# Optimization experiments

Hardware: AMD Instinct MI355X
Metric: run time of the kernel (lower is better)

The kernel has to match this reference:

```python
import jax, jax.numpy as jnp
import numpy as np

NEG = jnp.float32(-1e9)
N_PRE = 12000   # n_train_pre_nms (module default training=True)
N_POST = 2000   # n_train_post_nms
MIN_SIZE = 16.0
NMS_THRESH = 0.7


def _make_anchors(feat_size=64, stride=16):
    scales = np.array([128.0, 256.0, 512.0])
    ratios = np.array([0.5, 1.0, 2.0])
    ws = (scales[:, None] * np.sqrt(1.0 / ratios)[None, :]).reshape(-1)  # [9]
    hs = (scales[:, None] * np.sqrt(ratios)[None, :]).reshape(-1)        # [9]
    ctr = (np.arange(feat_size) + 0.5) * stride
    cy, cx = np.meshgrid(ctr, ctr, indexing='ij')
    cx = cx.reshape(-1, 1); cy = cy.reshape(-1, 1)                       # [4096,1]
    x1 = cx - 0.5 * ws[None, :]; y1 = cy - 0.5 * hs[None, :]
    x2 = cx + 0.5 * ws[None, :]; y2 = cy + 0.5 * hs[None, :]
    return np.stack([x1, y1, x2, y2], axis=-1).reshape(-1, 4).astype(np.float32)  # [36864,4]


def setup_inputs() -> dict:
    key = jax.random.key(0)
    k1, k2 = jax.random.split(key)
    anchors = jnp.asarray(_make_anchors())[None]            # [1, 36864, 4]
    B, N = 8, anchors.shape[1]
    pred_loc = jax.random.normal(k1, (B, N, 4), jnp.float32) * 0.2
    pred_obj = jax.random.normal(k2, (B, N, 2), jnp.float32)
    return {"img_height": 1024, "img_width": 1024,
            "anchor_boxes": anchors, "pred_loc": pred_loc, "pred_obj": pred_obj}


def _decode(anchors, loc, img_w, img_h):
    # anchors [N,4] (x1,y1,x2,y2), loc [N,4] (dx,dy,dw,dh)
    w = anchors[:, 2] - anchors[:, 0]
    h = anchors[:, 3] - anchors[:, 1]
    cx = anchors[:, 0] + 0.5 * w
    cy = anchors[:, 1] + 0.5 * h
    pcx = loc[:, 0] * w + cx
    pcy = loc[:, 1] * h + cy
    pw = jnp.exp(loc[:, 2]) * w
    ph = jnp.exp(loc[:, 3]) * h
    x1 = jnp.clip(pcx - 0.5 * pw, 0.0, img_w)
    y1 = jnp.clip(pcy - 0.5 * ph, 0.0, img_h)
    x2 = jnp.clip(pcx + 0.5 * pw, 0.0, img_w)
    y2 = jnp.clip(pcy + 0.5 * ph, 0.0, img_h)
    return jnp.stack([x1, y1, x2, y2], axis=-1)  # [N,4]


def _iou_one_vs_all(box, boxes):
    # box [4], boxes [M,4]
    ix1 = jnp.maximum(box[0], boxes[:, 0])
    iy1 = jnp.maximum(box[1], boxes[:, 1])
    ix2 = jnp.minimum(box[2], boxes[:, 2])
    iy2 = jnp.minimum(box[3], boxes[:, 3])
    inter = jnp.maximum(ix2 - ix1, 0.0) * jnp.maximum(iy2 - iy1, 0.0)
    a0 = (box[2] - box[0]) * (box[3] - box[1])
    a1 = (boxes[:, 2] - boxes[:, 0]) * (boxes[:, 3] - boxes[:, 1])
    return inter / jnp.maximum(a0 + a1 - inter, 1e-9)


def _greedy_nms(boxes, scores):
    # boxes [M,4], scores [M] (invalid entries already NEG). Selects the first
    # N_POST boxes kept by greedy IoU suppression (exactly torchvision nms +
    # [:n_post] truncation, since greedy NMS emits in descending-score order).
    def step(s, _):
        i = jnp.argmax(s)
        valid = s[i] > NEG * 0.5
        box = boxes[i]
        suppress = _iou_one_vs_all(box, boxes) > NMS_THRESH  # includes self
        s = jnp.where(suppress, NEG, s)
        return s, (box, valid)
    _, (kept, mask) = jax.lax.scan(step, scores, None, length=N_POST)
    return jnp.where(mask[:, None], kept, 0.0), mask  # [N_POST,4], [N_POST]


def reference(img_height, img_width, anchor_boxes, pred_loc, pred_obj):
    img_h = jnp.float32(img_height)
    img_w = jnp.float32(img_width)
    anchors = anchor_boxes[0]                                    # [N,4]
    scores = jax.nn.softmax(pred_obj, axis=2)[:, :, 1]           # [B,N]
    boxes = jax.vmap(lambda l: _decode(anchors, l, img_w, img_h))(pred_loc)  # [B,N,4]
    # min-size filter -> mask scores instead of dynamic filtering
    valid = jnp.all(boxes[..., 2:] - boxes[..., :2] >= MIN_SIZE, axis=-1)    # [B,N]
    scores = jnp.where(valid, scores, NEG)
    # descending sort + pre-NMS truncation == top_k
    top_s, top_i = jax.lax.top_k(scores, N_PRE)                  # [B,N_PRE]
    top_boxes = jnp.take_along_axis(boxes, top_i[..., None], axis=1)         # [B,N_PRE,4]
    kept_boxes, kept_mask = jax.vmap(_greedy_nms)(top_boxes, top_s)
    return kept_boxes, kept_mask  # [B,N_POST,4] padded, [B,N_POST] validity
```

## Files before the change

### kernel.cpp

```cpp
#include <hip/hip_runtime.h>

typedef unsigned long long u64;
typedef unsigned int u32;

#define B_SZ   8
#define N_ANC  36864
#define N_PRE  12000
#define N_POST 2000
#define SEG    2048
#define NSEG   6
#define MAXC   (SEG * NSEG)
#define NW     (SEG / 64)
#define NDW    (MAXC / 64)
#define NBLK   144

__device__ __forceinline__ float area_of(float4 p) {
  return __fmul_rn(__fsub_rn(p.z, p.x), __fsub_rn(p.w, p.y));
}

__device__ __forceinline__ bool iou_gt_a(float4 p, float4 q, float a0, float a1) {
  float ix1 = fmaxf(p.x, q.x), iy1 = fmaxf(p.y, q.y);
  float ix2 = fminf(p.z, q.z), iy2 = fminf(p.w, q.w);
  float iw = fmaxf(__fsub_rn(ix2, ix1), 0.0f);
  float ih = fmaxf(__fsub_rn(iy2, iy1), 0.0f);
  float inter = __fmul_rn(iw, ih);
  float den = fmaxf(__fsub_rn(__fadd_rn(a0, a1), inter), 1e-9f);
  return (inter / den) > 0.7f;
}

__device__ __forceinline__ void block_sync_lgkm() {
  __builtin_amdgcn_sched_barrier(0);
  asm volatile("s_waitcnt lgkmcnt(0)" ::: "memory");
  __builtin_amdgcn_s_barrier();
  __builtin_amdgcn_sched_barrier(0);
}

__global__ __launch_bounds__(256) void k_decode(
    const int* __restrict__ imh_p, const int* __restrict__ imw_p,
    const float* __restrict__ anchors, const float* __restrict__ loc,
    const float* __restrict__ obj, float4* __restrict__ boxes,
    u64* __restrict__ keys, u32* __restrict__ hist)
{
  __shared__ u32 lh[2048];
  int t = threadIdx.x;
#pragma unroll
  for (int i = 0; i < 8; ++i) lh[t + i * 256] = 0;
  __syncthreads();

  int n = blockIdx.x * 256 + t;
  int b = blockIdx.y;
  float a0 = anchors[n * 4 + 0], a1 = anchors[n * 4 + 1];
  float a2 = anchors[n * 4 + 2], a3 = anchors[n * 4 + 3];
  size_t off = (size_t)b * N_ANC + n;
  float l0 = loc[off * 4 + 0], l1 = loc[off * 4 + 1];
  float l2 = loc[off * 4 + 2], l3 = loc[off * 4 + 3];

  float w  = __fsub_rn(a2, a0);
  float h  = __fsub_rn(a3, a1);
  float cx = __fadd_rn(a0, __fmul_rn(0.5f, w));
  float cy = __fadd_rn(a1, __fmul_rn(0.5f, h));
  float pcx = __fadd_rn(__fmul_rn(l0, w), cx);
  float pcy = __fadd_rn(__fmul_rn(l1, h), cy);
  float pw  = __fmul_rn(expf(l2), w);
  float ph  = __fmul_rn(expf(l3), h);
  float imw = (float)imw_p[0], imh = (float)imh_p[0];
  float hx = __fmul_rn(0.5f, pw), hy = __fmul_rn(0.5f, ph);
  float x1 = fminf(fmaxf(__fsub_rn(pcx, hx), 0.0f), imw);
  float y1 = fminf(fmaxf(__fsub_rn(pcy, hy), 0.0f), imh);
  float x2 = fminf(fmaxf(__fadd_rn(pcx, hx), 0.0f), imw);
  float y2 = fminf(fmaxf(__fadd_rn(pcy, hy), 0.0f), imh);
  boxes[off] = make_float4(x1, y1, x2, y2);

  bool valid = (__fsub_rn(x2, x1) >= 16.0f) && (__fsub_rn(y2, y1) >= 16.0f);

  float o0 = obj[off * 2 + 0], o1 = obj[off * 2 + 1];
  float m  = fmaxf(o0, o1);
  float e0 = expf(__fsub_rn(o0, m));
  float e1 = expf(__fsub_rn(o1, m));
  float s  = e1 / __fadd_rn(e0, e1);
  float sc = valid ? s : -1e9f;

  u32 u  = __float_as_uint(sc);
  u32 fk = (u & 0x80000000u) ? ~u : (u | 0x80000000u);
  u32 sk = ~fk;
  u64 key = ((u64)sk << 32) | (u32)n;
  keys[off] = key;
  atomicAdd(&lh[(u32)(key >> 53)], 1u);
  __syncthreads();
#pragma unroll
  for (int i = 0; i < 8; ++i) {
    u32 v = lh[t + i * 256];
    if (v) atomicAdd(&hist[b * 2048 + t + i * 256], v);
  }
}

__global__ __launch_bounds__(256) void k_pick1(
    const u32* __restrict__ hist, u32* __restrict__ T1, u32* __restrict__ Base1)
{
  int b = blockIdx.x, t = threadIdx.x;
  const u32* h = hist + b * 2048;
  __shared__ u32 part[256], pre[256];
  u32 loc[8], s = 0;
#pragma unroll
  for (int i = 0; i < 8; ++i) { loc[i] = h[t * 8 + i]; s += loc[i]; }
  part[t] = s;
  __syncthreads();
  if (t == 0) { u32 acc = 0; for (int i = 0; i < 256; ++i) { pre[i] = acc; acc += part[i]; } }
  __syncthreads();
  u32 acc = pre[t];
#pragma unroll
  for (int i = 0; i < 8; ++i) {
    u32 na = acc + loc[i];
    if (acc < N_PRE && na >= N_PRE) { T1[b] = (u32)(t * 8 + i); Base1[b] = acc; }
    acc = na;
  }
}

__global__ __launch_bounds__(256) void k_hist2(
    const u64* __restrict__ keys, const u32* __restrict__ T1,
    u32* __restrict__ hist)
{
  int b = blockIdx.y;
  u32 t1 = T1[b];
  __shared__ u32 lh[2048];
  int t = threadIdx.x;
#pragma unroll
  for (int i = 0; i < 8; ++i) lh[t + i * 256] = 0;
  __syncthreads();
#pragma unroll
  for (int k = 0; k < 4; ++k) {
    int i = blockIdx.x * 1024 + k * 256 + t;
    u64 key = keys[(size_t)b * N_ANC + i];
    if ((u32)(key >> 53) == t1) atomicAdd(&lh[(u32)(key >> 42) & 0x7FFu], 1u);
  }
  __syncthreads();
#pragma unroll
  for (int i = 0; i < 8; ++i) {
    u32 v = lh[t + i * 256];
    if (v) atomicAdd(&hist[b * 2048 + t + i * 256], v);
  }
}

__global__ __launch_bounds__(256) void k_pick2(
    const u32* __restrict__ hist, const u32* __restrict__ T1,
    const u32* __restrict__ Base1, u32* __restrict__ T2)
{
  int b = blockIdx.x, t = threadIdx.x;
  const u32* h = hist + b * 2048;
  __shared__ u32 part[256], pre[256];
  u32 loc[8], s = 0;
#pragma unroll
  for (int i = 0; i < 8; ++i) { loc[i] = h[t * 8 + i]; s += loc[i]; }
  part[t] = s;
  __syncthreads();
  if (t == 0) { u32 acc = Base1[b]; for (int i = 0; i < 256; ++i) { pre[i] = acc; acc += part[i]; } }
  __syncthreads();
  u32 acc = pre[t];
#pragma unroll
  for (int i = 0; i < 8; ++i) {
    u32 na = acc + loc[i];
    if (acc < N_PRE && na >= N_PRE) T2[b] = (T1[b] << 11) | (u32)(t * 8 + i);
    acc = na;
  }
}

__global__ __launch_bounds__(256) void k_count(
    const u64* __restrict__ keys, const u32* __restrict__ T2,
    u32* __restrict__ bcnt)
{
  int b = blockIdx.y;
  int i = blockIdx.x * 256 + threadIdx.x;
  u64 key = keys[(size_t)b * N_ANC + i];
  bool pred = (u32)(key >> 42) <= T2[b];
  u64 bal = __ballot(pred);
  __shared__ u32 wc[4];
  int wv = threadIdx.x >> 6, lane = threadIdx.x & 63;
  if (lane == 0) wc[wv] = (u32)__popcll(bal);
  __syncthreads();
  if (threadIdx.x == 0)
    bcnt[b * NBLK + blockIdx.x] = wc[0] + wc[1] + wc[2] + wc[3];
}

__global__ __launch_bounds__(256) void k_scatter(
    const u64* __restrict__ keys, const u32* __restrict__ T2,
    const u32* __restrict__ bcnt, u64* __restrict__ cand)
{
  int b = blockIdx.y, bx = blockIdx.x;
  int t = threadIdx.x;
  __shared__ u32 cnts[NBLK];
  __shared__ u32 wc[4];
  __shared__ u32 sbase;
  if (t < NBLK) cnts[t] = bcnt[b * NBLK + t];
  u64 key = keys[(size_t)b * N_ANC + bx * 256 + t];
  bool pred = (u32)(key >> 42) <= T2[b];
  u64 bal = __ballot(pred);
  int wv = t >> 6, lane = t & 63;
  if (lane == 0) wc[wv] = (u32)__popcll(bal);
  __syncthreads();
  if (t == 0) { u32 a = 0; for (int i = 0; i < bx; ++i) a += cnts[i]; sbase = a; }
  __syncthreads();
  u32 base = sbase;
  for (int w = 0; w < wv; ++w) base += wc[w];
  u32 rank = (u32)__popcll(bal & ((1ull << lane) - 1ull));
  if (pred) {
    u32 pos = base + rank;
    if (pos < MAXC) cand[(size_t)b * MAXC + pos] = key;
  }
}

#define SIDX(x) ((x) + ((x) >> 5))
__global__ __launch_bounds__(1024) void k_sort_tile(u64* __restrict__ a)
{
  int b = blockIdx.y, base = blockIdx.x * 2048;
  u64* p = a + (size_t)b * MAXC + base;
  __shared__ u64 lds[2048 + 64];
  int t = threadIdx.x;
  lds[SIDX(t)] = p[t];
  lds[SIDX(t + 1024)] = p[t + 1024];
  __syncthreads();
  for (int k = 2; k <= 2048; k <<= 1) {
    for (int j = k >> 1; j > 0; j >>= 1) {
      int i = ((t & ~(j - 1)) << 1) | (t & (j - 1));
      int l = i | j;
      bool asc = ((i & k) == 0);
      u64 x = lds[SIDX(i)], y = lds[SIDX(l)];
      if ((x > y) == asc) { lds[SIDX(i)] = y; lds[SIDX(l)] = x; }
      __syncthreads();
    }
  }
  p[t] = lds[SIDX(t)];
  p[t + 1024] = lds[SIDX(t + 1024)];
}

__global__ __launch_bounds__(256) void k_merge_gather(
    const u64* __restrict__ cand, const float4* __restrict__ boxes,
    float4* __restrict__ gbox, u64* __restrict__ deadm)
{
  int b = blockIdx.y;
  int p = blockIdx.x * 256 + threadIdx.x;
  const u64* cb = cand + (size_t)b * MAXC;
  u64 key = cb[p];
  int r = p >> 11;
  int rank = p & 2047;
#pragma unroll
  for (int s = 0; s < NSEG; ++s) {
    if (s == r) continue;
    const u64* run = cb + (s << 11);
    int lo = 0;
#pragma unroll
    for (int step = 2048; step >= 1; step >>= 1) {
      int np = lo + step;
      if (np <= 2048 && run[np - 1] < key) lo = np;
    }
    rank += lo;
  }
  bool valid = ((u32)(key >> 32) < 0x80000000u) && (rank < N_PRE);
  float4 bx = make_float4(0.f, 0.f, 0.f, 0.f);
  if (valid) bx = boxes[(size_t)b * N_ANC + (u32)key];
  gbox[(size_t)b * MAXC + rank] = bx;
  if (!valid) atomicOr(&deadm[b * NDW + (rank >> 6)], 1ull << (rank & 63));
}

__device__ __forceinline__ void segmask_tile(
    int b, int sg, int tile, const float4* __restrict__ gbox,
    u64* __restrict__ smask, u64* __restrict__ smaskT,
    float4* rbox, float* rarea, u64* diag)
{
  int r = tile, rg = 0;
  while (r >= 32 - rg) { r -= 32 - rg; ++rg; }
  int cw = rg + r;
  const float4* gb = gbox + (size_t)b * MAXC + sg * SEG;
  int t = threadIdx.x;
  if (t < 64) { float4 bx = gb[rg * 64 + t]; rbox[t] = bx; rarea[t] = area_of(bx); }
  __syncthreads();
  int wv = t >> 6, lane = t & 63;
  u64* srow = smask + (size_t)(b * NSEG + sg) * SEG * NW + (size_t)rg * 64 * NW;
  float4 cb4 = gb[cw * 64 + lane];
  float ca = area_of(cb4);
  bool isdiag = (cw == rg);
  for (int rr = wv * 16; rr < wv * 16 + 16; ++rr) {
    bool p = iou_gt_a(rbox[rr], cb4, rarea[rr], ca);
    if (isdiag) p = p && (lane > rr);
    u64 m = __ballot(p);
    if (lane == 0) { srow[(size_t)rr * NW + cw] = m; if (isdiag) diag[rr] = m; }
  }
  if (isdiag) {
    __syncthreads();
    if (t < 64) {
      u64 s = 0;
      for (int q = 0; q < 64; ++q) s |= ((diag[q] >> t) & 1ull) << q;
      smaskT[(size_t)(b * NSEG + sg) * SEG + rg * 64 + t] = s;
    }
  }
}

__global__ __launch_bounds__(256) void k_segmask01(
    const float4* __restrict__ gbox, u64* __restrict__ smask,
    u64* __restrict__ smaskT)
{
  __shared__ float4 rbox[64]; __shared__ float rarea[64]; __shared__ u64 diag[64];
  int b = blockIdx.y;
  int sg = blockIdx.x / 528, tile = blockIdx.x % 528;
  segmask_tile(b, sg, tile, gbox, smask, smaskT, rbox, rarea, diag);
}

__device__ __forceinline__ void cross_work(
    int b, int sg, int bx, const float4* __restrict__ gbox,
    const float4* __restrict__ keptb, const int* __restrict__ meta,
    u64* __restrict__ deadm, float4* kb, float* ka)
{
  int kc = bx >> 3, cbk = bx & 7;
  int nkept = meta[b * 8 + 0];
  int kbase = kc * 256;
  if (kbase >= nkept) return;
  int kcnt = min(256, nkept - kbase);
  int t = threadIdx.x;
  if (t < kcnt) {
    float4 k4 = keptb[(size_t)b * SEG + kbase + t];
    kb[t] = k4; ka[t] = area_of(k4);
  }
  __syncthreads();
  int gi = sg * SEG + cbk * 256 + t;
  float4 my = gbox[(size_t)b * MAXC + gi];
  float ma = area_of(my);
  bool sup = false;
  for (int kk = 0; kk < kcnt; ++kk) {
    if (iou_gt_a(kb[kk], my, ka[kk], ma)) { sup = true; break; }
  }
  u64 bm = __ballot(sup);
  if ((t & 63) == 0 && bm) atomicOr(&deadm[b * NDW + (gi >> 6)], bm);
}

__global__ __launch_bounds__(256) void k_cross(
    const float4* __restrict__ gbox, const float4* __restrict__ keptb,
    const int* __restrict__ meta, u64* __restrict__ deadm, int sg)
{
  int b = blockIdx.y;
  if (meta[b * 8 + 1]) return;
  __shared__ float4 kb[256]; __shared__ float ka[256];
  cross_work(b, sg, blockIdx.x, gbox, keptb, meta, deadm, kb, ka);
}

__global__ __launch_bounds__(256) void k_crossmask(
    const float4* __restrict__ gbox, const float4* __restrict__ keptb,
    const int* __restrict__ meta, u64* __restrict__ deadm,
    u64* __restrict__ smask, u64* __restrict__ smaskT, int sg)
{
  int b = blockIdx.y;
  if (meta[b * 8 + 1]) return;
  __shared__ float4 kb[256]; __shared__ float ka[256]; __shared__ u64 diag[64];
  if (blockIdx.x < 64) {
    cross_work(b, sg, blockIdx.x, gbox, keptb, meta, deadm, kb, ka);
  } else {
    segmask_tile(b, sg, blockIdx.x - 64, gbox, smask, smaskT,
                 kb, ka, diag);
  }
}

__global__ __launch_bounds__(1024) void k_walk(
    const float4* __restrict__ gbox, const u64* __restrict__ smask,
    const u64* __restrict__ smaskT, const u64* __restrict__ deadm,
    int* __restrict__ meta, float4* __restrict__ keptb,
    float* __restrict__ out, int sg)
{
  int b = blockIdx.x;
  if (meta[b * 8 + 1]) return;
  int t = threadIdx.x, wv = t >> 6, lane = t & 63;

  __shared__ u64 rowbuf[2][2048];
  __shared__ u64 stbuf[2][64];
  __shared__ float4 bbox[2][64];
  __shared__ u64 sdead[2];
  __shared__ u32 remv[64];
  __shared__ u32 klist[64];
  __shared__ int s_stop, s_nkept, s_kcnt;

  const u64* smb = smask + (size_t)(b * NSEG + sg) * SEG * NW;
  const u64* stb = smaskT + (size_t)(b * NSEG + sg) * SEG;
  const u64* dmb = deadm + b * NDW + sg * NW;
  const float4* gb = gbox + (size_t)b * MAXC + sg * SEG;
  float4* kbuf = keptb + (size_t)b * SEG;
  float4* ob = (float4*)(out + (size_t)b * N_POST * 4);
  float* om = out + (size_t)B_SZ * N_POST * 4 + (size_t)b * N_POST;

  {
    u64 a = smb[t], c = smb[t + 1024];
    u64 st_ = 0; float4 bb_ = make_float4(0.f, 0.f, 0.f, 0.f);
    if (t < 64) { st_ = stb[t]; bb_ = gb[t]; }
    u64 sd_ = (t == 0) ? dmb[0] : 0;
    rowbuf[0][t] = a;
    rowbuf[0][t + 1024] = c;
    if (t < 64) { stbuf[0][t] = st_; bbox[0][t] = bb_; remv[t] = 0; }
    if (t == 0) { sdead[0] = sd_; s_stop = 0; s_nkept = meta[b * 8 + 0]; }
  }
  int p0 = t - 64, p1 = p0 + 960, p2 = p0 + 1920;
  u64 Aa = 0, Ac = 0, Ae = 0, Ast = 0, Asd = 0;
  u64 Ba = 0, Bc = 0, Be = 0, Bst = 0, Bsd = 0;
  float4 Abb = make_float4(0.f, 0.f, 0.f, 0.f);
  float4 Bbb = make_float4(0.f, 0.f, 0.f, 0.f);
  if (wv > 0) {
    { const u64* src = smb + 2048;
      Aa = src[p0]; Ac = src[p1]; if (p0 < 128) Ae = src[p2];
      if (p0 < 64) { Ast = stb[64 + p0]; Abb = gb[64 + p0]; }
      if (t == 64) Asd = dmb[1]; }
    { const u64* src = smb + 2 * 2048;
      Ba = src[p0]; Bc = src[p1]; if (p0 < 128) Be = src[p2];
      if (p0 < 64) { Bst = stb[128 + p0]; Bbb = gb[128 + p0]; }
      if (t == 64) Bsd = dmb[2]; }
  }
  block_sync_lgkm();

  for (int g = 0; g < NW; ++g) {
    int cb = g & 1, nb = cb ^ 1;
    if (wv > 0) {
      bool useA = ((g & 1) == 0);
      if (g < NW - 1) {
        u64 wa = useA ? Aa : Ba, wc2 = useA ? Ac : Bc, we = useA ? Ae : Be;
        u64 wst = useA ? Ast : Bst, wsd = useA ? Asd : Bsd;
        float4 wbb = useA ? Abb : Bbb;
        rowbuf[nb][p0] = wa;
        rowbuf[nb][p1] = wc2;
        if (p0 < 128) rowbuf[nb][p2] = we;
        if (p0 < 64) { stbuf[nb][p0] = wst; bbox[nb][p0] = wbb; }
        if (t == 64) sdead[nb] = wsd;
      }
      if (g < NW - 3) {
        const u64* src = smb + (size_t)(g + 3) * 2048;
        u64 la = src[p0], lc = src[p1], le = (p0 < 128) ? src[p2] : 0;
        u64 lst = 0, lsd = 0;
        float4 lbb = make_float4(0.f, 0.f, 0.f, 0.f);
        if (p0 < 64) { lst = stb[(g + 3) * 64 + p0]; lbb = gb[(g + 3) * 64 + p0]; }
        if (t == 64) lsd = dmb[g + 3];
        if (useA) { Aa = la; Ac = lc; Ae = le; Ast = lst; Abb = lbb; Asd = lsd; }
        else      { Ba = la; Bc = lc; Be = le; Bst = lst; Bbb = lbb; Bsd = lsd; }
      }
    } else {
      int l = lane;
      u64 S = stbuf[cb][l];
      u64 remg = ((u64)remv[2 * g + 1] << 32) | remv[2 * g];
      u64 avail = ~(remg | sdead[cb]);
      u64 km = 0;
      while (avail) {
        bool al = (avail >> l) & 1;
        u64 newk = __ballot(al && (S & avail) == 0ull);
        u64 nd   = __ballot(al && (S & newk) != 0ull);
        km |= newk;
        avail &= ~(newk | nd);
      }
      int nk0 = s_nkept;
      int rem = N_POST - nk0;
      int kc = __popcll(km);
      bool stop = (kc >= rem);
      int rank = __popcll(km & ((1ull << l) - 1ull));
      if (((km >> l) & 1) && rank < rem) {
        float4 bx = bbox[cb][l];
        kbuf[nk0 + rank] = bx;
        ob[nk0 + rank] = bx;
        om[nk0 + rank] = 1.0f;
        klist[rank] = (u32)l;
      }
      if (l == 0) {
        int eff = stop ? rem : kc;
        s_kcnt = eff;
        s_nkept = nk0 + eff;
        if (stop) s_stop = 1;
      }
    }
    block_sync_lgkm();
    if (s_stop) break;
    if (g < NW - 1) {
      int kcnt = s_kcnt;
      if (kcnt) {
        u32* rb32 = (u32*)rowbuf[cb];
        for (int i = t; i < kcnt * 64; i += 1024) {
          int kk = i >> 6, w = i & 63;
          if ((w >> 1) > g) {
            u32 v = rb32[klist[kk] * 64 + w];
            if (v) atomicOr(&remv[w], v);
          }
        }
      }
    }
    block_sync_lgkm();
  }
  int nk = s_nkept;
  bool fin = s_stop || (sg == NSEG - 1);
  if (t == 0) { meta[b * 8 + 0] = nk; if (fin) meta[b * 8 + 1] = 1; }
  if (fin) {
    float4 zero = make_float4(0.f, 0.f, 0.f, 0.f);
    for (int i = nk + t; i < N_POST; i += 1024) { ob[i] = zero; om[i] = 0.0f; }
  }
}

extern "C" void kernel_launch(void* const* d_in, const int* in_sizes, int n_in,
                              void* d_out, int out_size, void* d_ws, size_t ws_size,
                              hipStream_t stream)
{
  const int*   imh     = (const int*)d_in[0];
  const int*   imw     = (const int*)d_in[1];
  const float* anchors = (const float*)d_in[2];
  const float* loc     = (const float*)d_in[3];
  const float* obj     = (const float*)d_in[4];
  float* out = (float*)d_out;

  char* ws = (char*)d_ws;
  size_t off = 0;
  float4* boxes = (float4*)(ws + off); off += (size_t)B_SZ * N_ANC * 16;
  u64*    keys  = (u64*)   (ws + off); off += (size_t)B_SZ * N_ANC * 8;
  u64*    cand  = (u64*)   (ws + off); off += (size_t)B_SZ * MAXC * 8;
  float4* gbox  = (float4*)(ws + off); off += (size_t)B_SZ * MAXC * 16;
  float4* keptb = (float4*)(ws + off); off += (size_t)B_SZ * SEG * 16;
  off = (off + 255) & ~(size_t)255;
  char*   zr    = ws + off;
  u32*    hist1 = (u32*)(zr);
  u32*    hist2 = (u32*)(zr + 65536);
  u32*    T1    = (u32*)(zr + 131072);
  u32*    Base1 = (u32*)(zr + 131072 + 32);
  u32*    T2    = (u32*)(zr + 131072 + 64);
  int*    meta  = (int*)(zr + 131072 + 128);
  u64*    deadm = (u64*)(zr + 131072 + 128 + 256);
  u32*    bcnt  = (u32*)(zr + 131072 + 128 + 256 + (size_t)B_SZ * NDW * 8);
  size_t  zr_sz = 131072 + 128 + 256 + (size_t)B_SZ * NDW * 8
                + (size_t)B_SZ * NBLK * 4;
  off += (zr_sz + 255) & ~(size_t)255;
  u64*    smask  = (u64*)(ws + off); off += (size_t)B_SZ * NSEG * SEG * NW * 8;
  u64*    smaskT = (u64*)(ws + off); off += (size_t)B_SZ * NSEG * SEG * 8;

  hipMemsetAsync(zr, 0, zr_sz, stream);
  hipMemsetAsync(cand, 0xFF, (size_t)B_SZ * MAXC * 8, stream);

  k_decode<<<dim3(NBLK, B_SZ), 256, 0, stream>>>(imh, imw, anchors, loc, obj,
                                                 boxes, keys, hist1);
  k_pick1<<<B_SZ, 256, 0, stream>>>(hist1, T1, Base1);
  k_hist2<<<dim3(36, B_SZ), 256, 0, stream>>>(keys, T1, hist2);
  k_pick2<<<B_SZ, 256, 0, stream>>>(hist2, T1, Base1, T2);

  k_count<<<dim3(NBLK, B_SZ), 256, 0, stream>>>(keys, T2, bcnt);
  k_scatter<<<dim3(NBLK, B_SZ), 256, 0, stream>>>(keys, T2, bcnt, cand);

  k_sort_tile<<<dim3(NSEG, B_SZ), 1024, 0, stream>>>(cand);
  k_merge_gather<<<dim3(MAXC / 256, B_SZ), 256, 0, stream>>>(cand, boxes, gbox, deadm);

  k_segmask01<<<dim3(1056, B_SZ), 256, 0, stream>>>(gbox, smask, smaskT);

  k_walk<<<B_SZ, 1024, 0, stream>>>(gbox, smask, smaskT, deadm, meta, keptb, out, 0);
  k_cross<<<dim3(64, B_SZ), 256, 0, stream>>>(gbox, keptb, meta, deadm, 1);
  k_walk<<<B_SZ, 1024, 0, stream>>>(gbox, smask, smaskT, deadm, meta, keptb, out, 1);
  for (int sg = 2; sg < NSEG; ++sg) {
    k_crossmask<<<dim3(592, B_SZ), 256, 0, stream>>>(gbox, keptb, meta, deadm,
                                                     smask, smaskT, sg);
    k_walk<<<B_SZ, 1024, 0, stream>>>(gbox, smask, smaskT, deadm, meta, keptb, out, sg);
  }
}
```

Measured before the change: 225.1 us.

## Pipeline NMS walk: overlap suppression propagation with next group via triple buffering

The walk kernel now uses a triple-buffered row cache and splits the work across waves. Wave 0 does the greedy pick for group g. Waves 1-3 apply the previous group's kept-row suppression bits to later words, and waves 4-15 prefetch upcoming mask rows. Wave 0 ORs the previous group's contributions into the current word itself through a wave shuffle reduction, so the second barrier in each iteration can be removed. The aim is to halve synchronization per group and overlap the propagation work with the serial pick. The cost is more LDS use and fewer threads doing loads and propagation.

```diff
diff --git a/kernel.cpp b/kernel.cpp
--- a/kernel.cpp
+++ b/kernel.cpp
@@ -33,6 +33,12 @@
   asm volatile("s_waitcnt lgkmcnt(0)" ::: "memory");
   __builtin_amdgcn_s_barrier();
   __builtin_amdgcn_sched_barrier(0);
+}
+
+__device__ __forceinline__ u64 shfl64_xor(u64 v, int m) {
+  int lo = __shfl_xor((int)(u32)v, m, 64);
+  int hi = __shfl_xor((int)(u32)(v >> 32), m, 64);
+  return ((u64)(u32)hi << 32) | (u32)lo;
 }
 
 __global__ __launch_bounds__(256) void k_decode(
@@ -367,13 +373,14 @@
   if (meta[b * 8 + 1]) return;
   int t = threadIdx.x, wv = t >> 6, lane = t & 63;
 
-  __shared__ u64 rowbuf[2][2048];
-  __shared__ u64 stbuf[2][64];
-  __shared__ float4 bbox[2][64];
-  __shared__ u64 sdead[2];
+  __shared__ u64 rowbuf[3][2048];
+  __shared__ u64 stbuf[3][64];
+  __shared__ float4 bbox[3][64];
+  __shared__ u64 sdead[3];
   __shared__ u32 remv[64];
-  __shared__ u32 klist[64];
-  __shared__ int s_stop, s_nkept, s_kcnt;
+  __shared__ u32 klist[2][64];
+  __shared__ int kcnts[2];
+  __shared__ int s_stop, s_nkept;
 
   const u64* smb = smask + (size_t)(b * NSEG + sg) * SEG * NW;
   const u64* stb = smaskT + (size_t)(b * NSEG + sg) * SEG;
@@ -391,54 +398,64 @@
     rowbuf[0][t] = a;
     rowbuf[0][t + 1024] = c;
     if (t < 64) { stbuf[0][t] = st_; bbox[0][t] = bb_; remv[t] = 0; }
-    if (t == 0) { sdead[0] = sd_; s_stop = 0; s_nkept = meta[b * 8 + 0]; }
-  }
-  int p0 = t - 64, p1 = p0 + 960, p2 = p0 + 1920;
+    if (t == 0) { sdead[0] = sd_; s_stop = 0; s_nkept = meta[b * 8 + 0];
+                  kcnts[0] = 0; kcnts[1] = 0; }
+  }
+  int p0 = t - 256, p1 = p0 + 768, p2 = p0 + 1536;
   u64 Aa = 0, Ac = 0, Ae = 0, Ast = 0, Asd = 0;
   u64 Ba = 0, Bc = 0, Be = 0, Bst = 0, Bsd = 0;
   float4 Abb = make_float4(0.f, 0.f, 0.f, 0.f);
   float4 Bbb = make_float4(0.f, 0.f, 0.f, 0.f);
-  if (wv > 0) {
+  if (wv >= 4) {
     { const u64* src = smb + 2048;
-      Aa = src[p0]; Ac = src[p1]; if (p0 < 128) Ae = src[p2];
+      Aa = src[p0]; Ac = src[p1]; if (p0 < 512) Ae = src[p2];
       if (p0 < 64) { Ast = stb[64 + p0]; Abb = gb[64 + p0]; }
-      if (t == 64) Asd = dmb[1]; }
+      if (t == 256) Asd = dmb[1]; }
     { const u64* src = smb + 2 * 2048;
-      Ba = src[p0]; Bc = src[p1]; if (p0 < 128) Be = src[p2];
+      Ba = src[p0]; Bc = src[p1]; if (p0 < 512) Be = src[p2];
       if (p0 < 64) { Bst = stb[128 + p0]; Bbb = gb[128 + p0]; }
-      if (t == 64) Bsd = dmb[2]; }
+      if (t == 256) Bsd = dmb[2]; }
   }
   block_sync_lgkm();
 
   for (int g = 0; g < NW; ++g) {
-    int cb = g & 1, nb = cb ^ 1;
-    if (wv > 0) {
+    int rc = g % 3;
+    int rp = (g + 2) % 3;
+    int rn = (g + 1) % 3;
+    if (wv >= 4) {
       bool useA = ((g & 1) == 0);
       if (g < NW - 1) {
         u64 wa = useA ? Aa : Ba, wc2 = useA ? Ac : Bc, we = useA ? Ae : Be;
         u64 wst = useA ? Ast : Bst, wsd = useA ? Asd : Bsd;
         float4 wbb = useA ? Abb : Bbb;
-        rowbuf[nb][p0] = wa;
-        rowbuf[nb][p1] = wc2;
-        if (p0 < 128) rowbuf[nb][p2] = we;
-        if (p0 < 64) { stbuf[nb][p0] = wst; bbox[nb][p0] = wbb; }
-        if (t == 64) sdead[nb] = wsd;
+        rowbuf[rn][p0] = wa;
+        rowbuf[rn][p1] = wc2;
+        if (p0 < 512) rowbuf[rn][p2] = we;
+        if (p0 < 64) { stbuf[rn][p0] = wst; bbox[rn][p0] = wbb; }
+        if (t == 256) sdead[rn] = wsd;
       }
       if (g < NW - 3) {
         const u64* src = smb + (size_t)(g + 3) * 2048;
-        u64 la = src[p0], lc = src[p1], le = (p0 < 128) ? src[p2] : 0;
+        u64 la = src[p0], lc = src[p1], le = (p0 < 512) ? src[p2] : 0;
         u64 lst = 0, lsd = 0;
         float4 lbb = make_float4(0.f, 0.f, 0.f, 0.f);
         if (p0 < 64) { lst = stb[(g + 3) * 64 + p0]; lbb = gb[(g + 3) * 64 + p0]; }
-        if (t == 64) lsd = dmb[g + 3];
+        if (t == 256) lsd = dmb[g + 3];
         if (useA) { Aa = la; Ac = lc; Ae = le; Ast = lst; Abb = lbb; Asd = lsd; }
         else      { Ba = la; Bc = lc; Be = le; Bst = lst; Bbb = lbb; Bsd = lsd; }
       }
-    } else {
+    } else if (wv == 0) {
       int l = lane;
-      u64 S = stbuf[cb][l];
-      u64 remg = ((u64)remv[2 * g + 1] << 32) | remv[2 * g];
-      u64 avail = ~(remg | sdead[cb]);
+      u64 wprev = 0;
+      if (g > 0) {
+        int kcp = kcnts[(g - 1) & 1];
+        if (l < kcp) wprev = rowbuf[rp][klist[(g - 1) & 1][l] * NW + g];
+#pragma unroll
+        for (int m = 32; m >= 1; m >>= 1) wprev |= shfl64_xor(wprev, m);
+      }
+      u64 S = stbuf[rc][l];
+      u64 remg = (((u64)remv[2 * g + 1] << 32) | remv[2 * g]) | wprev;
+      u64 avail = ~(remg | sdead[rc]);
       u64 km = 0;
       while (avail) {
         bool al = (avail >> l) & 1;
@@ -453,35 +470,36 @@
       bool stop = (kc >= rem);
       int rank = __popcll(km & ((1ull << l) - 1ull));
       if (((km >> l) & 1) && rank < rem) {
-        float4 bx = bbox[cb][l];
+        float4 bx = bbox[rc][l];
         kbuf[nk0 + rank] = bx;
         ob[nk0 + rank] = bx;
         om[nk0 + rank] = 1.0f;
-        klist[rank] = (u32)l;
+        klist[g & 1][rank] = (u32)l;
       }
       if (l == 0) {
         int eff = stop ? rem : kc;
-        s_kcnt = eff;
+        kcnts[g & 1] = eff;
         s_nkept = nk0 + eff;
         if (stop) s_stop = 1;
+      }
+    } else {
+      if (g > 0) {
+        int kcp = kcnts[(g - 1) & 1];
+        if (kcp) {
+          const u32* rb32 = (const u32*)rowbuf[rp];
+          const u32* kl = klist[(g - 1) & 1];
+          for (int i = t - 64; i < kcp * 64; i += 192) {
+            int kk = i >> 6, w = i & 63;
+            if ((w >> 1) > g) {
+              u32 v = rb32[kl[kk] * 64 + w];
+              if (v) atomicOr(&remv[w], v);
+            }
+          }
+        }
       }
     }
     block_sync_lgkm();
     if (s_stop) break;
-    if (g < NW - 1) {
-      int kcnt = s_kcnt;
-      if (kcnt) {
-        u32* rb32 = (u32*)rowbuf[cb];
-        for (int i = t; i < kcnt * 64; i += 1024) {
-          int kk = i >> 6, w = i & 63;
-          if ((w >> 1) > g) {
-            u32 v = rb32[klist[kk] * 64 + w];
-            if (v) atomicOr(&remv[w], v);
-          }
-        }
-      }
-    }
-    block_sync_lgkm();
   }
   int nk = s_nkept;
   bool fin = s_stop || (sg == NSEG - 1);
```

After: 248.7 us. +10.5%, slower.
